# Optimization experiments

Measured on AMD Instinct MI355X. Metric: run time of the kernel, lower is better.

Reference implementation:

```python
import jax, jax.numpy as jnp
import numpy as np

N_GENE, N_CT, N_REF, N_SAMPLE = 50000, 64, 16, 1024

def setup_inputs() -> dict:
    key = jax.random.key(0)
    k1, k2, k3, k4, k5, k6 = jax.random.split(key, 6)
    x = jax.random.normal(k1, (N_GENE * N_CT * N_REF,), dtype=jnp.float32)
    idx = jax.random.randint(k2, (N_CT, N_GENE), 0, N_CT * N_GENE)
    # RefCombLayer weight: uniform around 1/n_ref
    num = 1.0 / N_REF
    w_ref = jax.random.uniform(k3, (N_REF * N_CT,), minval=num - num / 5, maxval=num + num / 5, dtype=jnp.float32)
    # CelltypeScaleLayer weight: normal(1.0, 0.1)
    w_ct = 1.0 + 0.1 * jax.random.normal(k4, (N_CT,), dtype=jnp.float32)
    # StretchLayer weight: normal(1.0, 0.1)
    w_stretch = 1.0 + 0.1 * jax.random.normal(k5, (N_GENE,), dtype=jnp.float32)
    # conv1 kernel: (n_sample, 1, n_kernel), normal(1/n_ct, 0.25/n_ct)
    conv_w = (1.0 / N_CT) + (0.25 / N_CT) * jax.random.normal(k6, (N_SAMPLE, 1, N_CT), dtype=jnp.float32)
    return {"x": x, "idx": idx, "w_ref": w_ref, "w_ct": w_ct,
            "w_stretch": w_stretch, "conv_w": conv_w,
            "N_batch": 1, "N_feature": N_GENE * N_CT}


def reference(x, idx, w_ref, w_ct, w_stretch, conv_w, N_batch, N_feature):
    # RefCombLayer: elementwise mul by per-gene-tiled ref weights
    y = x * jnp.tile(w_ref, N_GENE)                       # [n_gene*n_ct*n_ref]
    # SliceSumLayer: sum over n_ref slices
    y0 = y.reshape(N_CT * N_GENE, N_REF).sum(axis=1)      # [n_ct*n_gene]
    # CelltypeScaleLayer: gather per cell type, scale, flatten transposed
    z = y0[idx] * w_ct[:, None]                           # [n_ct, n_gene]
    y1 = z.T.reshape(-1)                                  # [n_gene*n_ct], gene-major
    # StretchLayer: per-gene weight repeated n_ct times
    y2 = y1 * jnp.repeat(w_stretch, N_CT)                 # [n_gene*n_ct]
    # Conv1d(1, n_sample, kernel=n_ct, stride=n_ct) == per-gene dot with kernel
    yk = y2.reshape(N_GENE, N_CT)                         # [n_gene, n_ct]
    out = jnp.einsum('gk,sk->sg', yk, conv_w[:, 0, :])    # [n_sample, n_gene]
    return (out, y0, y1, y2)
```

## Files before the change

### kernel.cpp

```cpp
#include <hip/hip_runtime.h>

#define NG 50000
#define NCT 64
#define NREF 16
#define NS 1024
#define N0 (NCT * NG)

#define OFF_Y0 ((size_t)NS * NG)
#define OFF_Y1 (OFF_Y0 + N0)
#define OFF_Y2 (OFF_Y1 + N0)

typedef __attribute__((ext_vector_type(8))) short bf16x8;
typedef __attribute__((ext_vector_type(4))) float f32x4;

__device__ __forceinline__ unsigned short f2bf(float f) {
    union { float f; unsigned u; } v; v.f = f;
    unsigned r = v.u + 0x7fff + ((v.u >> 16) & 1);
    return (unsigned short)(r >> 16);
}
__device__ __forceinline__ float bf2f(unsigned short b) {
    union { float f; unsigned u; } v; v.u = ((unsigned)b) << 16;
    return v.f;
}

__global__ __launch_bounds__(256) void k_y0(const float* __restrict__ x,
                                            const float* __restrict__ w_ref,
                                            float* __restrict__ y0) {
    __shared__ float4 wl[256];
    const int tid = threadIdx.x;
    wl[tid] = reinterpret_cast<const float4*>(w_ref)[tid];
    __syncthreads();
    const int row = tid & 63;
    const float4 w0 = wl[row * 4 + 0];
    const float4 w1 = wl[row * 4 + 1];
    const float4 w2 = wl[row * 4 + 2];
    const float4 w3 = wl[row * 4 + 3];
    const float4* x4 = reinterpret_cast<const float4*>(x);
    const size_t stride = (size_t)gridDim.x * 256;
    for (size_t j = (size_t)blockIdx.x * 256 + tid; j < (size_t)N0; j += stride) {
        const float4* xp = x4 + j * 4;
        float4 a = xp[0], b = xp[1], c = xp[2], d = xp[3];
        float s = a.x * w0.x + a.y * w0.y + a.z * w0.z + a.w * w0.w
                + b.x * w1.x + b.y * w1.y + b.z * w1.z + b.w * w1.w
                + c.x * w2.x + c.y * w2.y + c.z * w2.z + c.w * w2.w
                + d.x * w3.x + d.y * w3.y + d.z * w3.z + d.w * w3.w;
        y0[j] = s;
    }
}

__global__ __launch_bounds__(256) void k_gather(const float* __restrict__ y0,
                                                const int* __restrict__ idx,
                                                const float* __restrict__ w_ct,
                                                const float* __restrict__ w_stretch,
                                                float* __restrict__ y1,
                                                float* __restrict__ y2) {
    __shared__ float T[64][65];
    const int tid = threadIdx.x;
    const int g0 = blockIdx.x * 64;
#pragma unroll
    for (int k = 0; k < 16; ++k) {
        int lin = k * 256 + tid;
        int c = lin >> 6, gl = lin & 63;
        int g = g0 + gl;
        float t = 0.f;
        if (g < NG) t = y0[idx[c * NG + g]];
        T[c][gl] = t;
    }
    __syncthreads();
#pragma unroll
    for (int k = 0; k < 16; ++k) {
        int lin = k * 256 + tid;
        int gl = lin >> 6, c = lin & 63;
        int g = g0 + gl;
        if (g < NG) {
            float t = T[c][gl];
            float v1 = t * w_ct[c];
            float v2 = v1 * w_stretch[g];
            size_t o = (size_t)g * 64 + c;
            y1[o] = v1;
            y2[o] = v2;
        }
    }
}

#define STILE 128
__global__ __launch_bounds__(256) void k_conv(const float* __restrict__ y2,
                                              const float* __restrict__ cw,
                                              float* __restrict__ out) {
    __shared__ unsigned short Yhi[64 * 72];
    __shared__ unsigned short Ylo[64 * 72];
    __shared__ unsigned short Whi[STILE * 72];
    __shared__ unsigned short Wlo[STILE * 72];
    const int tid = threadIdx.x;
    const int g0 = blockIdx.x * 64;
    const int s0 = blockIdx.y * STILE;

#pragma unroll
    for (int it = 0; it < 4; ++it) {
        int e0 = (it * 256 + tid) * 4;
        int gp = e0 >> 6;
        int cp = e0 & 63;
        float4 v = make_float4(0.f, 0.f, 0.f, 0.f);
        if (g0 + gp < NG) v = *reinterpret_cast<const float4*>(y2 + (size_t)(g0 + gp) * 64 + cp);
        unsigned short h0 = f2bf(v.x), h1 = f2bf(v.y), h2 = f2bf(v.z), h3 = f2bf(v.w);
        int base = gp * 72 + cp;
        Yhi[base + 0] = h0; Yhi[base + 1] = h1; Yhi[base + 2] = h2; Yhi[base + 3] = h3;
        Ylo[base + 0] = f2bf(v.x - bf2f(h0));
        Ylo[base + 1] = f2bf(v.y - bf2f(h1));
        Ylo[base + 2] = f2bf(v.z - bf2f(h2));
        Ylo[base + 3] = f2bf(v.w - bf2f(h3));
    }
#pragma unroll
    for (int it = 0; it < 8; ++it) {
        int e0 = (it * 256 + tid) * 4;
        int sp = e0 >> 6;
        int cp = e0 & 63;
        float4 v = *reinterpret_cast<const float4*>(cw + (size_t)(s0 + sp) * 64 + cp);
        unsigned short h0 = f2bf(v.x), h1 = f2bf(v.y), h2 = f2bf(v.z), h3 = f2bf(v.w);
        int base = sp * 72 + cp;
        Whi[base + 0] = h0; Whi[base + 1] = h1; Whi[base + 2] = h2; Whi[base + 3] = h3;
        Wlo[base + 0] = f2bf(v.x - bf2f(h0));
        Wlo[base + 1] = f2bf(v.y - bf2f(h1));
        Wlo[base + 2] = f2bf(v.z - bf2f(h2));
        Wlo[base + 3] = f2bf(v.w - bf2f(h3));
    }
    __syncthreads();

    const int lane = tid & 63;
    const int wid  = tid >> 6;
    const int l15  = lane & 15;
    const int l4   = lane >> 4;
    const int nb   = wid * 32;

    bf16x8 Bh[2][2], Bl[2][2];
#pragma unroll
    for (int n = 0; n < 2; ++n) {
        int srow = nb + n * 16 + l15;
#pragma unroll
        for (int ks = 0; ks < 2; ++ks) {
            int koff = ks * 32 + l4 * 8;
            Bh[n][ks] = *reinterpret_cast<const bf16x8*>(&Whi[srow * 72 + koff]);
            Bl[n][ks] = *reinterpret_cast<const bf16x8*>(&Wlo[srow * 72 + koff]);
        }
    }

    f32x4 acc[4][2];
#pragma unroll
    for (int m = 0; m < 4; ++m)
#pragma unroll
        for (int n = 0; n < 2; ++n) acc[m][n] = (f32x4){0.f, 0.f, 0.f, 0.f};

#pragma unroll
    for (int m = 0; m < 4; ++m) {
        int grow = m * 16 + l15;
        bf16x8 Ah[2], Al[2];
#pragma unroll
        for (int ks = 0; ks < 2; ++ks) {
            int koff = ks * 32 + l4 * 8;
            Ah[ks] = *reinterpret_cast<const bf16x8*>(&Yhi[grow * 72 + koff]);
            Al[ks] = *reinterpret_cast<const bf16x8*>(&Ylo[grow * 72 + koff]);
        }
#pragma unroll
        for (int n = 0; n < 2; ++n) {
#pragma unroll
            for (int ks = 0; ks < 2; ++ks) {
                acc[m][n] = __builtin_amdgcn_mfma_f32_16x16x32_bf16(Ah[ks], Bh[n][ks], acc[m][n], 0, 0, 0);
                acc[m][n] = __builtin_amdgcn_mfma_f32_16x16x32_bf16(Ah[ks], Bl[n][ks], acc[m][n], 0, 0, 0);
                acc[m][n] = __builtin_amdgcn_mfma_f32_16x16x32_bf16(Al[ks], Bh[n][ks], acc[m][n], 0, 0, 0);
            }
        }
    }

#pragma unroll
    for (int m = 0; m < 4; ++m) {
        int g4 = g0 + m * 16 + l4 * 4;
        if (g4 < NG) {
#pragma unroll
            for (int n = 0; n < 2; ++n) {
                int s = s0 + nb + n * 16 + l15;
                *reinterpret_cast<f32x4*>(out + (size_t)s * NG + g4) = acc[m][n];
            }
        }
    }
}

extern "C" void kernel_launch(void* const* d_in, const int* in_sizes, int n_in,
                              void* d_out, int out_size, void* d_ws, size_t ws_size,
                              hipStream_t stream) {
    const float* x         = (const float*)d_in[0];
    const int*   idx       = (const int*)d_in[1];
    const float* w_ref     = (const float*)d_in[2];
    const float* w_ct      = (const float*)d_in[3];
    const float* w_stretch = (const float*)d_in[4];
    const float* conv_w    = (const float*)d_in[5];

    float* out = (float*)d_out;
    float* y0  = out + OFF_Y0;
    float* y1  = out + OFF_Y1;
    float* y2  = out + OFF_Y2;

    k_y0<<<2048, 256, 0, stream>>>(x, w_ref, y0);
    k_gather<<<(NG + 63) / 64, 256, 0, stream>>>(y0, idx, w_ct, w_stretch, y1, y2);
    k_conv<<<dim3((NG + 63) / 64, NS / STILE), 256, 0, stream>>>(y2, conv_w, out);
}
```

Baseline: 184.9 us.

## Fuse gather/scale into conv kernel, loop over sample tiles, add nontemporal loads/stores

Merges the gather/scale kernel into the conv kernel. The y2 tile is split into bf16 hi/lo parts straight in shared memory instead of being re-read from global memory, and each block now loops over all sample tiles, reusing its A fragments held in registers. The gather is restructured to issue all index loads first and then all value loads, and nontemporal hints are added to the large streaming loads and stores. The trade-off is fewer blocks (one per gene tile instead of eight), so less parallelism, and the conv weights are re-converted on every iteration.

```diff
diff --git a/kernel.cpp b/kernel.cpp
--- a/kernel.cpp
+++ b/kernel.cpp
@@ -26,20 +26,23 @@
 __global__ __launch_bounds__(256) void k_y0(const float* __restrict__ x,
                                             const float* __restrict__ w_ref,
                                             float* __restrict__ y0) {
-    __shared__ float4 wl[256];
+    __shared__ f32x4 wl[256];
     const int tid = threadIdx.x;
-    wl[tid] = reinterpret_cast<const float4*>(w_ref)[tid];
+    wl[tid] = reinterpret_cast<const f32x4*>(w_ref)[tid];
     __syncthreads();
     const int row = tid & 63;
-    const float4 w0 = wl[row * 4 + 0];
-    const float4 w1 = wl[row * 4 + 1];
-    const float4 w2 = wl[row * 4 + 2];
-    const float4 w3 = wl[row * 4 + 3];
-    const float4* x4 = reinterpret_cast<const float4*>(x);
+    const f32x4 w0 = wl[row * 4 + 0];
+    const f32x4 w1 = wl[row * 4 + 1];
+    const f32x4 w2 = wl[row * 4 + 2];
+    const f32x4 w3 = wl[row * 4 + 3];
+    const f32x4* x4 = reinterpret_cast<const f32x4*>(x);
     const size_t stride = (size_t)gridDim.x * 256;
     for (size_t j = (size_t)blockIdx.x * 256 + tid; j < (size_t)N0; j += stride) {
-        const float4* xp = x4 + j * 4;
-        float4 a = xp[0], b = xp[1], c = xp[2], d = xp[3];
+        const f32x4* xp = x4 + j * 4;
+        f32x4 a = __builtin_nontemporal_load(xp + 0);
+        f32x4 b = __builtin_nontemporal_load(xp + 1);
+        f32x4 c = __builtin_nontemporal_load(xp + 2);
+        f32x4 d = __builtin_nontemporal_load(xp + 3);
         float s = a.x * w0.x + a.y * w0.y + a.z * w0.z + a.w * w0.w
                 + b.x * w1.x + b.y * w1.y + b.z * w1.z + b.w * w1.w
                 + c.x * w2.x + c.y * w2.y + c.z * w2.z + c.w * w2.w
@@ -48,81 +51,61 @@
     }
 }
 
-__global__ __launch_bounds__(256) void k_gather(const float* __restrict__ y0,
-                                                const int* __restrict__ idx,
-                                                const float* __restrict__ w_ct,
-                                                const float* __restrict__ w_stretch,
-                                                float* __restrict__ y1,
-                                                float* __restrict__ y2) {
-    __shared__ float T[64][65];
+#define STILE 128
+__global__ __launch_bounds__(256) void k_fused(const float* __restrict__ y0,
+                                               const int* __restrict__ idx,
+                                               const float* __restrict__ w_ct,
+                                               const float* __restrict__ w_stretch,
+                                               const float* __restrict__ cw,
+                                               float* __restrict__ y1,
+                                               float* __restrict__ y2,
+                                               float* __restrict__ out) {
+    __shared__ unsigned short Yhi[64 * 72];
+    __shared__ unsigned short Ylo[64 * 72];
+    __shared__ char Rbuf[2 * STILE * 72 * 2];
+    float* T = reinterpret_cast<float*>(Rbuf);
+    unsigned short* Whi = reinterpret_cast<unsigned short*>(Rbuf);
+    unsigned short* Wlo = Whi + STILE * 72;
+
     const int tid = threadIdx.x;
     const int g0 = blockIdx.x * 64;
+
+    int ids[16];
 #pragma unroll
     for (int k = 0; k < 16; ++k) {
         int lin = k * 256 + tid;
         int c = lin >> 6, gl = lin & 63;
-        int g = g0 + gl;
-        float t = 0.f;
-        if (g < NG) t = y0[idx[c * NG + g]];
-        T[c][gl] = t;
+        int gc = min(g0 + gl, NG - 1);
+        ids[k] = idx[c * NG + gc];
+    }
+    float vals[16];
+#pragma unroll
+    for (int k = 0; k < 16; ++k) vals[k] = y0[ids[k]];
+#pragma unroll
+    for (int k = 0; k < 16; ++k) {
+        int lin = k * 256 + tid;
+        int c = lin >> 6, gl = lin & 63;
+        T[c * 65 + gl] = vals[k];
     }
     __syncthreads();
+
 #pragma unroll
     for (int k = 0; k < 16; ++k) {
         int lin = k * 256 + tid;
         int gl = lin >> 6, c = lin & 63;
         int g = g0 + gl;
+        float t = T[c * 65 + gl];
+        float v1 = t * w_ct[c];
+        float v2 = v1 * w_stretch[min(g, NG - 1)];
+        int base = gl * 72 + c;
+        unsigned short h = f2bf(v2);
+        Yhi[base] = h;
+        Ylo[base] = f2bf(v2 - bf2f(h));
         if (g < NG) {
-            float t = T[c][gl];
-            float v1 = t * w_ct[c];
-            float v2 = v1 * w_stretch[g];
             size_t o = (size_t)g * 64 + c;
-            y1[o] = v1;
-            y2[o] = v2;
-        }
-    }
-}
-
-#define STILE 128
-__global__ __launch_bounds__(256) void k_conv(const float* __restrict__ y2,
-                                              const float* __restrict__ cw,
-                                              float* __restrict__ out) {
-    __shared__ unsigned short Yhi[64 * 72];
-    __shared__ unsigned short Ylo[64 * 72];
-    __shared__ unsigned short Whi[STILE * 72];
-    __shared__ unsigned short Wlo[STILE * 72];
-    const int tid = threadIdx.x;
-    const int g0 = blockIdx.x * 64;
-    const int s0 = blockIdx.y * STILE;
-
-#pragma unroll
-    for (int it = 0; it < 4; ++it) {
-        int e0 = (it * 256 + tid) * 4;
-        int gp = e0 >> 6;
-        int cp = e0 & 63;
-        float4 v = make_float4(0.f, 0.f, 0.f, 0.f);
-        if (g0 + gp < NG) v = *reinterpret_cast<const float4*>(y2 + (size_t)(g0 + gp) * 64 + cp);
-        unsigned short h0 = f2bf(v.x), h1 = f2bf(v.y), h2 = f2bf(v.z), h3 = f2bf(v.w);
-        int base = gp * 72 + cp;
-        Yhi[base + 0] = h0; Yhi[base + 1] = h1; Yhi[base + 2] = h2; Yhi[base + 3] = h3;
-        Ylo[base + 0] = f2bf(v.x - bf2f(h0));
-        Ylo[base + 1] = f2bf(v.y - bf2f(h1));
-        Ylo[base + 2] = f2bf(v.z - bf2f(h2));
-        Ylo[base + 3] = f2bf(v.w - bf2f(h3));
-    }
-#pragma unroll
-    for (int it = 0; it < 8; ++it) {
-        int e0 = (it * 256 + tid) * 4;
-        int sp = e0 >> 6;
-        int cp = e0 & 63;
-        float4 v = *reinterpret_cast<const float4*>(cw + (size_t)(s0 + sp) * 64 + cp);
-        unsigned short h0 = f2bf(v.x), h1 = f2bf(v.y), h2 = f2bf(v.z), h3 = f2bf(v.w);
-        int base = sp * 72 + cp;
-        Whi[base + 0] = h0; Whi[base + 1] = h1; Whi[base + 2] = h2; Whi[base + 3] = h3;
-        Wlo[base + 0] = f2bf(v.x - bf2f(h0));
-        Wlo[base + 1] = f2bf(v.y - bf2f(h1));
-        Wlo[base + 2] = f2bf(v.z - bf2f(h2));
-        Wlo[base + 3] = f2bf(v.w - bf2f(h3));
+            __builtin_nontemporal_store(v1, y1 + o);
+            __builtin_nontemporal_store(v2, y2 + o);
+        }
     }
     __syncthreads();
 
@@ -132,55 +115,76 @@
     const int l4   = lane >> 4;
     const int nb   = wid * 32;
 
-    bf16x8 Bh[2][2], Bl[2][2];
-#pragma unroll
-    for (int n = 0; n < 2; ++n) {
-        int srow = nb + n * 16 + l15;
+    bf16x8 Ah[4][2], Al[4][2];
+#pragma unroll
+    for (int m = 0; m < 4; ++m) {
+        int grow = m * 16 + l15;
 #pragma unroll
         for (int ks = 0; ks < 2; ++ks) {
             int koff = ks * 32 + l4 * 8;
-            Bh[n][ks] = *reinterpret_cast<const bf16x8*>(&Whi[srow * 72 + koff]);
-            Bl[n][ks] = *reinterpret_cast<const bf16x8*>(&Wlo[srow * 72 + koff]);
-        }
-    }
-
-    f32x4 acc[4][2];
-#pragma unroll
-    for (int m = 0; m < 4; ++m)
-#pragma unroll
-        for (int n = 0; n < 2; ++n) acc[m][n] = (f32x4){0.f, 0.f, 0.f, 0.f};
-
-#pragma unroll
-    for (int m = 0; m < 4; ++m) {
-        int grow = m * 16 + l15;
-        bf16x8 Ah[2], Al[2];
-#pragma unroll
-        for (int ks = 0; ks < 2; ++ks) {
-            int koff = ks * 32 + l4 * 8;
-            Ah[ks] = *reinterpret_cast<const bf16x8*>(&Yhi[grow * 72 + koff]);
-            Al[ks] = *reinterpret_cast<const bf16x8*>(&Ylo[grow * 72 + koff]);
-        }
+            Ah[m][ks] = *reinterpret_cast<const bf16x8*>(&Yhi[grow * 72 + koff]);
+            Al[m][ks] = *reinterpret_cast<const bf16x8*>(&Ylo[grow * 72 + koff]);
+        }
+    }
+
+    for (int s0 = 0; s0 < NS; s0 += STILE) {
+#pragma unroll
+        for (int it = 0; it < 8; ++it) {
+            int e0 = (it * 256 + tid) * 4;
+            int sp = e0 >> 6;
+            int cp = e0 & 63;
+            f32x4 v = *reinterpret_cast<const f32x4*>(cw + (size_t)(s0 + sp) * 64 + cp);
+            unsigned short h0 = f2bf(v.x), h1 = f2bf(v.y), h2 = f2bf(v.z), h3 = f2bf(v.w);
+            int base = sp * 72 + cp;
+            Whi[base + 0] = h0; Whi[base + 1] = h1; Whi[base + 2] = h2; Whi[base + 3] = h3;
+            Wlo[base + 0] = f2bf(v.x - bf2f(h0));
+            Wlo[base + 1] = f2bf(v.y - bf2f(h1));
+            Wlo[base + 2] = f2bf(v.z - bf2f(h2));
+            Wlo[base + 3] = f2bf(v.w - bf2f(h3));
+        }
+        __syncthreads();
+
+        bf16x8 Bh[2][2], Bl[2][2];
 #pragma unroll
         for (int n = 0; n < 2; ++n) {
+            int srow = nb + n * 16 + l15;
 #pragma unroll
             for (int ks = 0; ks < 2; ++ks) {
-                acc[m][n] = __builtin_amdgcn_mfma_f32_16x16x32_bf16(Ah[ks], Bh[n][ks], acc[m][n], 0, 0, 0);
-                acc[m][n] = __builtin_amdgcn_mfma_f32_16x16x32_bf16(Ah[ks], Bl[n][ks], acc[m][n], 0, 0, 0);
-                acc[m][n] = __builtin_amdgcn_mfma_f32_16x16x32_bf16(Al[ks], Bh[n][ks], acc[m][n], 0, 0, 0);
+                int koff = ks * 32 + l4 * 8;
+                Bh[n][ks] = *reinterpret_cast<const bf16x8*>(&Whi[srow * 72 + koff]);
+                Bl[n][ks] = *reinterpret_cast<const bf16x8*>(&Wlo[srow * 72 + koff]);
             }
         }
-    }
-
-#pragma unroll
-    for (int m = 0; m < 4; ++m) {
-        int g4 = g0 + m * 16 + l4 * 4;
-        if (g4 < NG) {
-#pragma unroll
-            for (int n = 0; n < 2; ++n) {
-                int s = s0 + nb + n * 16 + l15;
-                *reinterpret_cast<f32x4*>(out + (size_t)s * NG + g4) = acc[m][n];
+
+        f32x4 acc[4][2];
+#pragma unroll
+        for (int m = 0; m < 4; ++m)
+#pragma unroll
+            for (int n = 0; n < 2; ++n) acc[m][n] = (f32x4){0.f, 0.f, 0.f, 0.f};
+
+#pragma unroll
+        for (int m = 0; m < 4; ++m)
+#pragma unroll
+            for (int n = 0; n < 2; ++n)
+#pragma unroll
+                for (int ks = 0; ks < 2; ++ks) {
+                    acc[m][n] = __builtin_amdgcn_mfma_f32_16x16x32_bf16(Ah[m][ks], Bh[n][ks], acc[m][n], 0, 0, 0);
+                    acc[m][n] = __builtin_amdgcn_mfma_f32_16x16x32_bf16(Ah[m][ks], Bl[n][ks], acc[m][n], 0, 0, 0);
+                    acc[m][n] = __builtin_amdgcn_mfma_f32_16x16x32_bf16(Al[m][ks], Bh[n][ks], acc[m][n], 0, 0, 0);
+                }
+
+#pragma unroll
+        for (int m = 0; m < 4; ++m) {
+            int g4 = g0 + m * 16 + l4 * 4;
+            if (g4 < NG) {
+#pragma unroll
+                for (int n = 0; n < 2; ++n) {
+                    int s = s0 + nb + n * 16 + l15;
+                    __builtin_nontemporal_store(acc[m][n], reinterpret_cast<f32x4*>(out + (size_t)s * NG + g4));
+                }
             }
         }
+        __syncthreads();
     }
 }
 
@@ -200,6 +204,5 @@
     float* y2  = out + OFF_Y2;
 
     k_y0<<<2048, 256, 0, stream>>>(x, w_ref, y0);
-    k_gather<<<(NG + 63) / 64, 256, 0, stream>>>(y0, idx, w_ct, w_stretch, y1, y2);
-    k_conv<<<dim3((NG + 63) / 64, NS / STILE), 256, 0, stream>>>(y2, conv_w, out);
-}
+    k_fused<<<(NG + 63) / 64, 256, 0, stream>>>(y0, idx, w_ct, w_stretch, conv_w, y1, y2, out);
+}
```

Result: faster. 180.2 us (-2.5%).
